# Kernel tuning notes

Hardware: AMD Instinct MI355X
Metric: run time of the kernel (lower is better)

The kernel has to match this reference:

```python
import jax, jax.numpy as jnp
import numpy as np

IN_F = 4096
OUT_F = 4096
P_FWD = 0.95
P_BWD = 0.90
BATCH = 4096


def setup_inputs() -> dict:
    rng = np.random.default_rng(0)
    # kaiming_uniform_(a=sqrt(5)) on (OUT_F, IN_F) => bound = 1/sqrt(fan_in)
    bound = 1.0 / np.sqrt(IN_F)
    weight = rng.uniform(-bound, bound, size=(OUT_F, IN_F)).astype(np.float32)
    aw = np.abs(weight)
    # compute_mask: |w| >= p-quantile of |w|
    thr_f = np.quantile(aw, P_FWD)
    thr_b = np.quantile(aw, P_BWD)
    mask_f = aw >= thr_f
    mask_jb = (aw >= thr_b) & ~mask_f  # B \ A (justbwd)
    rf, cf = np.nonzero(mask_f)
    rj, cj = np.nonzero(mask_jb)
    rows = np.concatenate([rf, rj]).astype(np.int32)
    cols = np.concatenate([cf, cj]).astype(np.int32)
    # active_fwd_weights = [weight[idx_fwd], zeros(len(justbwd))]
    vals = np.concatenate([weight[rf, cf],
                           np.zeros(len(rj), np.float32)]).astype(np.float32)
    bias = rng.uniform(-bound, bound, size=(OUT_F,)).astype(np.float32)
    inputs = jax.random.normal(jax.random.key(0), (BATCH, IN_F), dtype=jnp.float32)
    return {
        "inputs": inputs,
        "vals": jnp.asarray(vals),
        "rows": jnp.asarray(rows),
        "cols": jnp.asarray(cols),
        "bias": jnp.asarray(bias),
    }


def reference(inputs, vals, rows, cols, bias):
    # COO spmm: y = spmm(indices, vals, OUT_F, IN_F, inputs^T)^T + bias.
    # Scatter COO values into the (OUT_F, IN_F) weight, then one GEMM;
    # this matches the sparse matmul math exactly (indices are unique).
    W = jnp.zeros((OUT_F, IN_F), dtype=vals.dtype).at[rows, cols].add(vals)
    return inputs @ W.T + bias  # [BATCH, OUT_F]
```

## Files before the change

### kernel.cpp

```cpp
#include <hip/hip_runtime.h>
#include <hip/hip_bf16.h>
#include <stdint.h>

typedef unsigned short u16;

#define IN_F  4096
#define OUT_F 4096
#define BATCH 4096

__device__ __forceinline__ u16 f2bf(float f) {
    uint32_t u = __float_as_uint(f);
    uint32_t r = u + 0x7FFFu + ((u >> 16) & 1u);
    return (u16)(r >> 16);
}

__global__ void zero_w_kernel(u16* __restrict__ Wb) {
    size_t tid = (size_t)blockIdx.x * blockDim.x + threadIdx.x;
    uint4 z = {0u, 0u, 0u, 0u};
    *(uint4*)(Wb + tid * 8) = z;
}

__global__ void convert_x_kernel(const float* __restrict__ X, u16* __restrict__ Xb) {
    size_t tid = (size_t)blockIdx.x * blockDim.x + threadIdx.x;
    const float4* p = (const float4*)(X + tid * 8);
    float4 a = p[0];
    float4 b = p[1];
    uint4 o;
    o.x = (uint32_t)f2bf(a.x) | ((uint32_t)f2bf(a.y) << 16);
    o.y = (uint32_t)f2bf(a.z) | ((uint32_t)f2bf(a.w) << 16);
    o.z = (uint32_t)f2bf(b.x) | ((uint32_t)f2bf(b.y) << 16);
    o.w = (uint32_t)f2bf(b.z) | ((uint32_t)f2bf(b.w) << 16);
    *(uint4*)(Xb + tid * 8) = o;
}

__global__ void scatter_kernel(const float* __restrict__ vals,
                               const int* __restrict__ rows,
                               const int* __restrict__ cols,
                               u16* __restrict__ Wb, int nnz) {
    int i = blockIdx.x * blockDim.x + threadIdx.x;
    if (i < nnz) {
        Wb[(size_t)rows[i] * IN_F + cols[i]] = f2bf(vals[i]);
    }
}

typedef __bf16 bf16x8 __attribute__((ext_vector_type(8)));
typedef float  f32x4  __attribute__((ext_vector_type(4)));

#define NPH   (IN_F / 32)
#define SLOTW 16384

__device__ __forceinline__ void gld_lds16(const void* g, void* l) {
    __builtin_amdgcn_global_load_lds(
        (const __attribute__((address_space(1))) uint32_t*)(uintptr_t)g,
        (__attribute__((address_space(3))) uint32_t*)(uintptr_t)l,
        16, 0, 0);
}

__global__ __launch_bounds__(512, 2)
void gemm_kernel(const u16* __restrict__ Xb, const u16* __restrict__ Wb,
                 const float* __restrict__ bias, float* __restrict__ out) {
    extern __shared__ __align__(16) u16 lds[];

    const int tid  = threadIdx.x;
    const int lane = tid & 63;
    const int w    = tid >> 6;
    const int wr   = w >> 2;
    const int wc   = w & 3;

    const int bid = blockIdx.x;
    const int swz = (bid & 7) * 32 + (bid >> 3);
    const int br  = (swz >> 4) * 256;
    const int bc  = (swz & 15) * 256;

    const int l2 = lane >> 2;
    const int sw = (lane & 3) ^ ((lane >> 3) & 3);
    const u16* asrc[4];
    int        adst[4];
#pragma unroll
    for (int i = 0; i < 4; ++i) {
        const int c = w * 4 + i;
        if (c < 16) {
            asrc[i] = Xb + (size_t)(br + c * 16 + l2) * IN_F + sw * 8;
            adst[i] = c * 512;
        } else {
            asrc[i] = Wb + (size_t)(bc + (c - 16) * 16 + l2) * IN_F + sw * 8;
            adst[i] = 8192 + (c - 16) * 512;
        }
    }

    const int sp = (lane >> 4) ^ ((lane >> 1) & 3);
    int aoff[8], boff[4];
#pragma unroll
    for (int m = 0; m < 8; ++m)
        aoff[m] = (wr * 128 + m * 16 + (lane & 15)) * 32 + sp * 8;
#pragma unroll
    for (int n = 0; n < 4; ++n)
        boff[n] = 8192 + (wc * 64 + n * 16 + (lane & 15)) * 32 + sp * 8;

    f32x4 acc[8][4] = {};

#pragma unroll
    for (int kh = 0; kh < 3; ++kh) {
        const int sbase = (kh & 3) * SLOTW;
#pragma unroll
        for (int i = 0; i < 4; ++i)
            gld_lds16(asrc[i] + kh * 32, lds + sbase + adst[i]);
    }

#define PHASE(G, VMLIT, STG)                                                    \
    do {                                                                        \
        asm volatile("s_waitcnt vmcnt(" #VMLIT ")" ::: "memory");               \
        __builtin_amdgcn_s_barrier();                                           \
        if (STG) {                                                              \
            const int kh = (G) + 3;                                             \
            const int sbase = (kh & 3) * SLOTW;                                 \
            _Pragma("unroll")                                                   \
            for (int i = 0; i < 4; ++i)                                         \
                gld_lds16(asrc[i] + (size_t)kh * 32, lds + sbase + adst[i]);    \
        }                                                                       \
        const u16* sl = lds + ((G) & 3) * SLOTW;                                \
        bf16x8 a[8], b[4];                                                      \
        _Pragma("unroll")                                                       \
        for (int m = 0; m < 8; ++m)                                             \
            a[m] = __builtin_bit_cast(bf16x8, *(const uint4*)(sl + aoff[m]));   \
        _Pragma("unroll")                                                       \
        for (int n = 0; n < 4; ++n)                                             \
            b[n] = __builtin_bit_cast(bf16x8, *(const uint4*)(sl + boff[n]));   \
        __builtin_amdgcn_s_setprio(1);                                          \
        _Pragma("unroll")                                                       \
        for (int m = 0; m < 8; ++m)                                             \
            _Pragma("unroll")                                                   \
            for (int n = 0; n < 4; ++n)                                         \
                acc[m][n] = __builtin_amdgcn_mfma_f32_16x16x32_bf16(            \
                    a[m], b[n], acc[m][n], 0, 0, 0);                            \
        __builtin_amdgcn_s_setprio(0);                                          \
    } while (0)

    for (int g = 0; g < NPH - 3; ++g)
        PHASE(g, 8, true);
    PHASE(NPH - 3, 8, false);
    PHASE(NPH - 2, 4, false);
    PHASE(NPH - 1, 0, false);
#undef PHASE

    const int cl = lane & 15;
    const int rg = (lane >> 4) * 4;
#pragma unroll
    for (int n = 0; n < 4; ++n) {
        const int col = bc + wc * 64 + n * 16 + cl;
        const float bv = bias[col];
#pragma unroll
        for (int m = 0; m < 8; ++m) {
            const int row0 = br + wr * 128 + m * 16 + rg;
#pragma unroll
            for (int j = 0; j < 4; ++j)
                out[(size_t)(row0 + j) * OUT_F + col] = acc[m][n][j] + bv;
        }
    }
}

extern "C" void kernel_launch(void* const* d_in, const int* in_sizes, int n_in,
                              void* d_out, int out_size, void* d_ws, size_t ws_size,
                              hipStream_t stream) {
    const float* X    = (const float*)d_in[0];
    const float* vals = (const float*)d_in[1];
    const int*   rows = (const int*)d_in[2];
    const int*   cols = (const int*)d_in[3];
    const float* bias = (const float*)d_in[4];
    float*       out  = (float*)d_out;
    const int    nnz  = in_sizes[1];

    u16* Wb = (u16*)d_ws;
    u16* Xb = (u16*)((char*)d_ws + (size_t)OUT_F * IN_F * 2);

    zero_w_kernel<<<8192, 256, 0, stream>>>(Wb);
    convert_x_kernel<<<8192, 256, 0, stream>>>(X, Xb);
    scatter_kernel<<<(nnz + 255) / 256, 256, 0, stream>>>(vals, rows, cols, Wb, nnz);

    static bool attr_set = false;
    (void)hipFuncSetAttribute((const void*)gemm_kernel,
                              hipFuncAttributeMaxDynamicSharedMemorySize, 131072);
    (void)attr_set;

    gemm_kernel<<<dim3(256), dim3(512), 131072, stream>>>(Xb, Wb, bias, out);
}
```

Before: 147.5 us.

## Split GEMM k-phase into two interleaved slices and merge prep kernels

The zero-fill and X-to-bf16 conversion kernels are merged into one launch so a kernel boundary disappears. Each k-phase of the GEMM main loop is split into two half-slices. Each half loads four A fragments, issues two of the four global-to-LDS prefetches, hits an extra barrier and then runs sixteen MFMAs. This spreads memory issue across the MFMA work and halves the A register footprint, at the cost of two extra barriers per phase.

```diff
diff --git a/kernel.cpp b/kernel.cpp
--- a/kernel.cpp
+++ b/kernel.cpp
@@ -14,23 +14,24 @@
     return (u16)(r >> 16);
 }
 
-__global__ void zero_w_kernel(u16* __restrict__ Wb) {
-    size_t tid = (size_t)blockIdx.x * blockDim.x + threadIdx.x;
-    uint4 z = {0u, 0u, 0u, 0u};
-    *(uint4*)(Wb + tid * 8) = z;
-}
-
-__global__ void convert_x_kernel(const float* __restrict__ X, u16* __restrict__ Xb) {
-    size_t tid = (size_t)blockIdx.x * blockDim.x + threadIdx.x;
-    const float4* p = (const float4*)(X + tid * 8);
-    float4 a = p[0];
-    float4 b = p[1];
-    uint4 o;
-    o.x = (uint32_t)f2bf(a.x) | ((uint32_t)f2bf(a.y) << 16);
-    o.y = (uint32_t)f2bf(a.z) | ((uint32_t)f2bf(a.w) << 16);
-    o.z = (uint32_t)f2bf(b.x) | ((uint32_t)f2bf(b.y) << 16);
-    o.w = (uint32_t)f2bf(b.z) | ((uint32_t)f2bf(b.w) << 16);
-    *(uint4*)(Xb + tid * 8) = o;
+__global__ void prep_kernel(const float* __restrict__ X, u16* __restrict__ Xb,
+                            u16* __restrict__ Wb) {
+    if (blockIdx.x < 8192) {
+        size_t tid = (size_t)blockIdx.x * blockDim.x + threadIdx.x;
+        uint4 z = {0u, 0u, 0u, 0u};
+        *(uint4*)(Wb + tid * 8) = z;
+    } else {
+        size_t tid = (size_t)(blockIdx.x - 8192) * blockDim.x + threadIdx.x;
+        const float4* p = (const float4*)(X + tid * 8);
+        float4 a = p[0];
+        float4 b = p[1];
+        uint4 o;
+        o.x = (uint32_t)f2bf(a.x) | ((uint32_t)f2bf(a.y) << 16);
+        o.y = (uint32_t)f2bf(a.z) | ((uint32_t)f2bf(a.w) << 16);
+        o.z = (uint32_t)f2bf(b.x) | ((uint32_t)f2bf(b.y) << 16);
+        o.w = (uint32_t)f2bf(b.z) | ((uint32_t)f2bf(b.w) << 16);
+        *(uint4*)(Xb + tid * 8) = o;
+    }
 }
 
 __global__ void scatter_kernel(const float* __restrict__ vals,
@@ -107,41 +108,56 @@
             gld_lds16(asrc[i] + kh * 32, lds + sbase + adst[i]);
     }
 
-#define PHASE(G, VMLIT, STG)                                                    \
+#define SLICE(G, VMLIT, STG)                                                    \
     do {                                                                        \
         asm volatile("s_waitcnt vmcnt(" #VMLIT ")" ::: "memory");               \
         __builtin_amdgcn_s_barrier();                                           \
-        if (STG) {                                                              \
-            const int kh = (G) + 3;                                             \
-            const int sbase = (kh & 3) * SLOTW;                                 \
-            _Pragma("unroll")                                                   \
-            for (int i = 0; i < 4; ++i)                                         \
-                gld_lds16(asrc[i] + (size_t)kh * 32, lds + sbase + adst[i]);    \
-        }                                                                       \
         const u16* sl = lds + ((G) & 3) * SLOTW;                                \
-        bf16x8 a[8], b[4];                                                      \
+        const int  sb = (((G) + 3) & 3) * SLOTW;                                \
+        bf16x8 a[4], b[4];                                                      \
         _Pragma("unroll")                                                       \
-        for (int m = 0; m < 8; ++m)                                             \
+        for (int m = 0; m < 4; ++m)                                             \
             a[m] = __builtin_bit_cast(bf16x8, *(const uint4*)(sl + aoff[m]));   \
         _Pragma("unroll")                                                       \
         for (int n = 0; n < 4; ++n)                                             \
             b[n] = __builtin_bit_cast(bf16x8, *(const uint4*)(sl + boff[n]));   \
+        if (STG) {                                                              \
+            gld_lds16(asrc[0] + (size_t)((G) + 3) * 32, lds + sb + adst[0]);    \
+            gld_lds16(asrc[1] + (size_t)((G) + 3) * 32, lds + sb + adst[1]);    \
+        }                                                                       \
+        __builtin_amdgcn_s_barrier();                                           \
         __builtin_amdgcn_s_setprio(1);                                          \
         _Pragma("unroll")                                                       \
-        for (int m = 0; m < 8; ++m)                                             \
+        for (int m = 0; m < 4; ++m)                                             \
             _Pragma("unroll")                                                   \
             for (int n = 0; n < 4; ++n)                                         \
                 acc[m][n] = __builtin_amdgcn_mfma_f32_16x16x32_bf16(            \
                     a[m], b[n], acc[m][n], 0, 0, 0);                            \
         __builtin_amdgcn_s_setprio(0);                                          \
+        _Pragma("unroll")                                                       \
+        for (int m = 0; m < 4; ++m)                                             \
+            a[m] = __builtin_bit_cast(bf16x8, *(const uint4*)(sl + aoff[m+4])); \
+        if (STG) {                                                              \
+            gld_lds16(asrc[2] + (size_t)((G) + 3) * 32, lds + sb + adst[2]);    \
+            gld_lds16(asrc[3] + (size_t)((G) + 3) * 32, lds + sb + adst[3]);    \
+        }                                                                       \
+        __builtin_amdgcn_s_barrier();                                           \
+        __builtin_amdgcn_s_setprio(1);                                          \
+        _Pragma("unroll")                                                       \
+        for (int m = 0; m < 4; ++m)                                             \
+            _Pragma("unroll")                                                   \
+            for (int n = 0; n < 4; ++n)                                         \
+                acc[m + 4][n] = __builtin_amdgcn_mfma_f32_16x16x32_bf16(        \
+                    a[m], b[n], acc[m + 4][n], 0, 0, 0);                        \
+        __builtin_amdgcn_s_setprio(0);                                          \
     } while (0)
 
     for (int g = 0; g < NPH - 3; ++g)
-        PHASE(g, 8, true);
-    PHASE(NPH - 3, 8, false);
-    PHASE(NPH - 2, 4, false);
-    PHASE(NPH - 1, 0, false);
-#undef PHASE
+        SLICE(g, 8, true);
+    SLICE(NPH - 3, 8, false);
+    SLICE(NPH - 2, 4, false);
+    SLICE(NPH - 1, 0, false);
+#undef SLICE
 
     const int cl = lane & 15;
     const int rg = (lane >> 4) * 4;
@@ -173,14 +189,11 @@
     u16* Wb = (u16*)d_ws;
     u16* Xb = (u16*)((char*)d_ws + (size_t)OUT_F * IN_F * 2);
 
-    zero_w_kernel<<<8192, 256, 0, stream>>>(Wb);
-    convert_x_kernel<<<8192, 256, 0, stream>>>(X, Xb);
+    prep_kernel<<<16384, 256, 0, stream>>>(X, Xb, Wb);
     scatter_kernel<<<(nnz + 255) / 256, 256, 0, stream>>>(vals, rows, cols, Wb, nnz);
 
-    static bool attr_set = false;
     (void)hipFuncSetAttribute((const void*)gemm_kernel,
                               hipFuncAttributeMaxDynamicSharedMemorySize, 131072);
-    (void)attr_set;
 
     gemm_kernel<<<dim3(256), dim3(512), 131072, stream>>>(Xb, Wb, bias, out);
 }
```

Measured after the change: 141.4 us. -4.2%, faster.
